# Optimization experiments

Hardware: AMD Instinct MI355X
Metric: run time of the kernel (lower is better)

Reference implementation:

```python
import jax, jax.numpy as jnp
import numpy as np

H = 256; NH = 4; DH = H // NH
NT, NS, NV = 4096, 2048, 1024
E1, E2, E3 = 65536, 16384, 32768
LN_EPS = 1e-5


def setup_inputs() -> dict:
    key = jax.random.key(0)
    ks = jax.random.split(key, 40)
    def nrm(i, shape):
        return jax.random.normal(ks[i], shape, jnp.float32) * 0.05
    inp = {
        "x_term": jax.random.normal(ks[0], (NT, H), jnp.float32),
        "x_symbol": jax.random.normal(ks[1], (NS, H), jnp.float32),
        "x_var": jax.random.normal(ks[2], (NV, H), jnp.float32),
        "ha_src": jax.random.randint(ks[3], (E1,), 0, NT),
        "ha_dst": jax.random.randint(ks[4], (E1,), 0, NT),
        "so_src": jax.random.randint(ks[5], (E2,), 0, NT),
        "so_dst": jax.random.randint(ks[6], (E2,), 0, NS),
        "vo_src": jax.random.randint(ks[7], (E3,), 0, NV),
        "vo_dst": jax.random.randint(ks[8], (E3,), 0, NT),
        # SAGEConv params for the 4 term-destination relations
        "Wl_rha": nrm(9, (H, H)),  "bl_rha": nrm(10, (H,)), "Wr_rha": nrm(11, (H, H)),
        "Wl_ha":  nrm(12, (H, H)), "bl_ha":  nrm(13, (H,)), "Wr_ha":  nrm(14, (H, H)),
        "Wl_rsym": nrm(15, (H, H)), "bl_rsym": nrm(16, (H,)), "Wr_rsym": nrm(17, (H, H)),
        "Wl_var": nrm(18, (H, H)), "bl_var": nrm(19, (H,)), "Wr_var": nrm(20, (H, H)),
        "ln_g": jnp.ones((H,), jnp.float32),
        "ln_b": jnp.zeros((H,), jnp.float32),
        "in_proj_w": nrm(21, (3 * H, H)),
        "in_proj_b": nrm(22, (3 * H,)),
        "out_proj_w": nrm(23, (H, H)),
        "out_proj_b": nrm(24, (H,)),
        "post_w": nrm(25, (H, H)),
        "post_b": nrm(26, (H,)),
    }
    return inp


def _sage(x_src, x_dst, src, dst, Wl, bl, Wr, num_dst):
    # PyG SAGEConv: lin_l(mean_j x_src[j]) + lin_r(x_dst)
    msg = x_src[src]                                            # [E, H] gather
    s = jax.ops.segment_sum(msg, dst, num_segments=num_dst)     # [N_dst, H] scatter-add
    cnt = jax.ops.segment_sum(jnp.ones((src.shape[0],), x_src.dtype), dst,
                              num_segments=num_dst)
    agg = s / jnp.maximum(cnt, 1.0)[:, None]
    return agg @ Wl.T + bl + x_dst @ Wr.T


def _layernorm(x, g, b):
    mu = jnp.mean(x, axis=-1, keepdims=True)
    var = jnp.mean(jnp.square(x - mu), axis=-1, keepdims=True)
    return (x - mu) * jax.lax.rsqrt(var + LN_EPS) * g + b


def _mha(x, in_w, in_b, out_w, out_b):
    # torch MultiheadAttention (eval, batch=1, self-attention)
    qkv = x @ in_w.T + in_b                       # [N, 3H]
    q, k, v = jnp.split(qkv, 3, axis=-1)
    def heads(t):
        return t.reshape(-1, NH, DH).transpose(1, 0, 2)  # [NH, N, DH]
    q, k, v = heads(q), heads(k), heads(v)
    scores = jnp.einsum("hqd,hkd->hqk", q, k) / np.sqrt(DH).astype(np.float32)
    a = jax.nn.softmax(scores, axis=-1)
    o = jnp.einsum("hqk,hkd->hqd", a, v)          # [NH, N, DH]
    o = o.transpose(1, 0, 2).reshape(-1, H)
    return o @ out_w.T + out_b


def reference(x_term, x_symbol, x_var,
              ha_src, ha_dst, so_src, so_dst, vo_src, vo_dst,
              Wl_rha, bl_rha, Wr_rha, Wl_ha, bl_ha, Wr_ha,
              Wl_rsym, bl_rsym, Wr_rsym, Wl_var, bl_var, Wr_var,
              ln_g, ln_b, in_proj_w, in_proj_b, out_proj_w, out_proj_b,
              post_w, post_b):
    nt = x_term.shape[0]
    # HeteroConv(aggr='sum') over the 4 relations whose destination is 'term'
    conv_term = (
        _sage(x_term, x_term, ha_dst, ha_src, Wl_rha, bl_rha, Wr_rha, nt)    # rev_has_arg
        + _sage(x_term, x_term, ha_src, ha_dst, Wl_ha, bl_ha, Wr_ha, nt)     # has_arg
        + _sage(x_symbol, x_term, so_dst, so_src, Wl_rsym, bl_rsym, Wr_rsym, nt)  # rev_symbol_of
        + _sage(x_var, x_term, vo_src, vo_dst, Wl_var, bl_var, Wr_var, nt)   # var_occurrence
    )
    term_out = _layernorm(conv_term + x_term, ln_g, ln_b)  # dropout is identity in eval
    attn_out = _mha(term_out, in_proj_w, in_proj_b, out_proj_w, out_proj_b)
    post = jax.nn.relu(attn_out @ post_w.T + post_b)
    term_final = post + term_out
    return term_final
```

## Files before the change

kernel.cpp:

```cpp
#include <hip/hip_runtime.h>
#include <hip/hip_bf16.h>

#define H 256
#define NT 4096
#define NHEAD 4
#define E1 65536
#define E2 16384
#define E3 32768
#define TOTE (2 * E1 + E2 + E3)
#define LN_EPS 1e-5f
#define SPLIT 4

typedef __hip_bfloat16 bf16;
typedef short bf16x8 __attribute__((ext_vector_type(8)));
typedef float f32x4 __attribute__((ext_vector_type(4)));

__device__ __forceinline__ float b2f(bf16 v) { return __bfloat162float(v); }
__device__ __forceinline__ float u2f(unsigned short u) {
    unsigned int x = ((unsigned int)u) << 16;
    return __uint_as_float(x);
}
__device__ __forceinline__ unsigned short f2u(float f) {
    bf16 h = __float2bfloat16(f);
    unsigned short v;
    __builtin_memcpy(&v, &h, 2);
    return v;
}
__device__ __forceinline__ float ldin(const void* p, size_t i, bool isbf) {
    return isbf ? b2f(((const bf16*)p)[i]) : ((const float*)p)[i];
}

__global__ __launch_bounds__(256) void k_init(float4* cnt4, int n4,
                                              const unsigned int* __restrict__ lng,
                                              unsigned int* __restrict__ flag) {
    int i = blockIdx.x * 256 + threadIdx.x;
    if (i == 0) *flag = (lng[0] == 0x3F803F80u) ? 1u : 0u;
    int stride = gridDim.x * 256;
    float4 z = make_float4(0.f, 0.f, 0.f, 0.f);
    for (; i < n4; i += stride) cnt4[i] = z;
}

__global__ __launch_bounds__(256) void k_count4(const int* __restrict__ s0, const int* __restrict__ s1,
                                                const int* __restrict__ s2, const int* __restrict__ s3,
                                                int* __restrict__ cnt) {
    int i = blockIdx.x * 256 + threadIdx.x;
    int r, e;
    if (i < E1) { r = 0; e = i; }
    else if (i < 2 * E1) { r = 1; e = i - E1; }
    else if (i < 2 * E1 + E2) { r = 2; e = i - 2 * E1; }
    else if (i < TOTE) { r = 3; e = i - 2 * E1 - E2; }
    else return;
    const int* s = (r == 0) ? s0 : (r == 1) ? s1 : (r == 2) ? s2 : s3;
    atomicAdd(&cnt[r * NT + s[e]], 1);
}

__global__ __launch_bounds__(256) void k_scan(const int* __restrict__ cnt, int* __restrict__ offs,
                                              int* __restrict__ cursor) {
    __shared__ int tot[256];
    int t = threadIdx.x, r = blockIdx.x;
    const int* c = cnt + r * NT;
    int* o = offs + r * (NT + 1);
    int* cur = cursor + r * NT;
    int base = t * 16;
    int local[16];
    int sum = 0;
#pragma unroll
    for (int j = 0; j < 16; j++) { local[j] = c[base + j]; sum += local[j]; }
    tot[t] = sum;
    __syncthreads();
    if (t == 0) {
        int run = 0;
        for (int i = 0; i < 256; i++) { int v = tot[i]; tot[i] = run; run += v; }
        o[NT] = run;
    }
    __syncthreads();
    int run = tot[t];
#pragma unroll
    for (int j = 0; j < 16; j++) { o[base + j] = run; cur[base + j] = run; run += local[j]; }
}

__global__ __launch_bounds__(256) void k_fill(const int* __restrict__ s0, const int* __restrict__ s1,
                                              const int* __restrict__ s2, const int* __restrict__ s3,
                                              const int* __restrict__ g0, const int* __restrict__ g1,
                                              const int* __restrict__ g2, const int* __restrict__ g3,
                                              int* __restrict__ cursor, int* __restrict__ csr) {
    int i = blockIdx.x * 256 + threadIdx.x;
    int r, e, rb;
    if (i < E1) { r = 0; e = i; rb = 0; }
    else if (i < 2 * E1) { r = 1; e = i - E1; rb = E1; }
    else if (i < 2 * E1 + E2) { r = 2; e = i - 2 * E1; rb = 2 * E1; }
    else if (i < TOTE) { r = 3; e = i - 2 * E1 - E2; rb = 2 * E1 + E2; }
    else return;
    const int* s = (r == 0) ? s0 : (r == 1) ? s1 : (r == 2) ? s2 : s3;
    const int* g = (r == 0) ? g0 : (r == 1) ? g1 : (r == 2) ? g2 : g3;
    int d = s[e];
    int pos = atomicAdd(&cursor[r * NT + d], 1);
    csr[rb + pos] = g[e];
}

__global__ __launch_bounds__(256) void k_gatherA(
    const void* __restrict__ x0, const void* __restrict__ x1,
    const void* __restrict__ x2, const void* __restrict__ x3,
    const int* __restrict__ offs, const int* __restrict__ csr,
    bf16* __restrict__ aggs, const unsigned int* __restrict__ flag) {
    int y = blockIdx.y;
    int i = blockIdx.x * 4 + (threadIdx.x >> 6);
    int lane = threadIdx.x & 63;
    bool isbf = (*flag != 0u);
    const void* x = (y == 0) ? x0 : (y == 1) ? x1 : (y == 2) ? x2 : x3;
    static const int rbase[4] = {0, E1, 2 * E1, 2 * E1 + E2};
    const int* o = offs + y * (NT + 1);
    const int* cs = csr + rbase[y];
    int b = o[i], e = o[i + 1];
    float ax = 0.f, ay = 0.f, az = 0.f, aw = 0.f;
    if (isbf) {
        for (int j = b; j < e; j++) {
            int s = cs[j];
            ushort4 u = *(const ushort4*)((const unsigned short*)x + (size_t)s * H + lane * 4);
            ax += u2f(u.x); ay += u2f(u.y); az += u2f(u.z); aw += u2f(u.w);
        }
    } else {
        for (int j = b; j < e; j++) {
            int s = cs[j];
            float4 v = *(const float4*)((const float*)x + (size_t)s * H + lane * 4);
            ax += v.x; ay += v.y; az += v.z; aw += v.w;
        }
    }
    float inv = 1.0f / fmaxf((float)(e - b), 1.0f);
    *(ushort4*)((unsigned short*)aggs + ((size_t)y * NT + i) * H + lane * 4) =
        make_ushort4(f2u(ax * inv), f2u(ay * inv), f2u(az * inv), f2u(aw * inv));
}

__global__ __launch_bounds__(256) void k_prepB(
    const void* __restrict__ Wl0, const void* __restrict__ Wl1,
    const void* __restrict__ Wl2, const void* __restrict__ Wl3,
    const void* __restrict__ Wr0, const void* __restrict__ Wr1,
    const void* __restrict__ Wr2, const void* __restrict__ Wr3,
    const void* __restrict__ b0, const void* __restrict__ b1,
    const void* __restrict__ b2, const void* __restrict__ b3,
    bf16* __restrict__ Bcat, float* __restrict__ bsum, const unsigned int* __restrict__ flag) {
    int idx = blockIdx.x * 256 + threadIdx.x;
    bool isbf = (*flag != 0u);
    int n = idx / 1280, k = idx % 1280;
    float v;
    if (k < 1024) {
        const void* W = (k < 256) ? Wl0 : (k < 512) ? Wl1 : (k < 768) ? Wl2 : Wl3;
        v = ldin(W, (size_t)n * 256 + (k & 255), isbf);
    } else {
        size_t o = (size_t)n * 256 + (k - 1024);
        v = ldin(Wr0, o, isbf) + ldin(Wr1, o, isbf) + ldin(Wr2, o, isbf) + ldin(Wr3, o, isbf);
    }
    ((unsigned short*)Bcat)[idx] = f2u(v);
    if (idx < 256)
        bsum[idx] = ldin(b0, idx, isbf) + ldin(b1, idx, isbf) + ldin(b2, idx, isbf) + ldin(b3, idx, isbf);
}

__global__ __launch_bounds__(256) void k_convln(
    const bf16* __restrict__ aggs, const bf16* __restrict__ Bcat, const float* __restrict__ bsum,
    const void* __restrict__ xt, const void* __restrict__ gw, const void* __restrict__ gb,
    bf16* __restrict__ term, const unsigned int* __restrict__ flag) {
    __shared__ unsigned short Asm[8 * 16 * 8];
    __shared__ unsigned short Bsm[8 * 256 * 8];
    __shared__ float redS[4][16];
    const bool isbf = (*flag != 0u);
    const int tid = threadIdx.x;
    const int w = tid >> 6, lane = tid & 63;
    const int col = lane & 15, quad = lane >> 4;
    const int m0 = blockIdx.x * 16;
    const int srow = tid & 63, skq = tid >> 6;

    f32x4 acc[4];
#pragma unroll
    for (int dt = 0; dt < 4; dt++) acc[dt] = (f32x4){0.f, 0.f, 0.f, 0.f};

    bf16x8 areg;
    bf16x8 breg[8];
    auto loadA = [&](int k0) {
        if (tid < 128) {
            int row = tid & 15, akq = tid >> 4;
            int k = k0 + akq * 8;
            if (k < 1024) {
                areg = *(const bf16x8*)((const unsigned short*)aggs +
                                        ((size_t)(k >> 8) * NT + m0 + row) * 256 + (k & 255));
            } else {
#pragma unroll
                for (int j = 0; j < 8; j++)
                    areg[j] = (short)f2u(ldin(xt, (size_t)(m0 + row) * 256 + (k - 1024) + j, isbf));
            }
        }
    };
    auto loadB = [&](int k0) {
#pragma unroll
        for (int t = 0; t < 4; t++)
#pragma unroll
            for (int kk = 0; kk < 2; kk++)
                breg[t * 2 + kk] = *(const bf16x8*)((const unsigned short*)Bcat +
                                       (size_t)(t * 64 + srow) * 1280 + k0 + (skq * 2 + kk) * 8);
    };

    loadA(0);
    loadB(0);
    for (int k0 = 0; k0 < 1280; k0 += 64) {
        __syncthreads();
        if (tid < 128) *(bf16x8*)&Asm[tid * 8] = areg;
#pragma unroll
        for (int t = 0; t < 4; t++)
#pragma unroll
            for (int kk = 0; kk < 2; kk++)
                *(bf16x8*)&Bsm[((skq * 2 + kk) * 256 + t * 64 + srow) * 8] = breg[t * 2 + kk];
        __syncthreads();
        if (k0 + 64 < 1280) { loadA(k0 + 64); loadB(k0 + 64); }
#pragma unroll
        for (int ch = 0; ch < 2; ch++) {
            bf16x8 a = *(const bf16x8*)&Asm[(((ch * 4 + quad) & 7) * 16 + col) * 8];
#pragma unroll
            for (int dt = 0; dt < 4; dt++) {
                bf16x8 b = *(const bf16x8*)&Bsm[((ch * 4 + quad) * 256 + w * 64 + dt * 16 + col) * 8];
                acc[dt] = __builtin_amdgcn_mfma_f32_16x16x32_bf16(a, b, acc[dt], 0, 0, 0);
            }
        }
    }

#pragma unroll
    for (int dt = 0; dt < 4; dt++) {
        int n = w * 64 + dt * 16 + col;
        float bsv = bsum[n];
#pragma unroll
        for (int r = 0; r < 4; r++) {
            int m = m0 + quad * 4 + r;
            acc[dt][r] += bsv + ldin(xt, (size_t)m * 256 + n, isbf);
        }
    }
    float mu[4], rs_[4];
#pragma unroll
    for (int r = 0; r < 4; r++) {
        float s = acc[0][r] + acc[1][r] + acc[2][r] + acc[3][r];
#pragma unroll
        for (int mk = 1; mk <= 8; mk <<= 1) s += __shfl_xor(s, mk);
        if (col == 0) redS[w][quad * 4 + r] = s;
    }
    __syncthreads();
#pragma unroll
    for (int r = 0; r < 4; r++) {
        int m = quad * 4 + r;
        mu[r] = (redS[0][m] + redS[1][m] + redS[2][m] + redS[3][m]) * (1.0f / 256.0f);
    }
    __syncthreads();
#pragma unroll
    for (int r = 0; r < 4; r++) {
        float s2 = 0.f;
#pragma unroll
        for (int dt = 0; dt < 4; dt++) {
            float d = acc[dt][r] - mu[r];
            s2 += d * d;
        }
#pragma unroll
        for (int mk = 1; mk <= 8; mk <<= 1) s2 += __shfl_xor(s2, mk);
        if (col == 0) redS[w][quad * 4 + r] = s2;
    }
    __syncthreads();
#pragma unroll
    for (int r = 0; r < 4; r++) {
        int m = quad * 4 + r;
        float var = (redS[0][m] + redS[1][m] + redS[2][m] + redS[3][m]) * (1.0f / 256.0f);
        rs_[r] = rsqrtf(var + LN_EPS);
    }
#pragma unroll
    for (int dt = 0; dt < 4; dt++) {
        int n = w * 64 + dt * 16 + col;
        float gv = ldin(gw, n, isbf), bv = ldin(gb, n, isbf);
#pragma unroll
        for (int r = 0; r < 4; r++) {
            int m = m0 + quad * 4 + r;
            term[(size_t)m * 256 + n] = __float2bfloat16((acc[dt][r] - mu[r]) * rs_[r] * gv + bv);
        }
    }
}

template <int AMODE, int EPI>
__global__ __launch_bounds__(256) void k_gemm(
    const void* __restrict__ A, const void* __restrict__ A2, const float* __restrict__ ml,
    const void* __restrict__ B, const void* __restrict__ bias,
    const bf16* __restrict__ resid, bf16* __restrict__ vt, void* __restrict__ outp,
    int M, int N, int K, const unsigned int* __restrict__ flag) {
    __shared__ unsigned short Asm[8 * 64 * 8];
    __shared__ unsigned short Bsm[8 * 64 * 8];
    const bool isbf = (*flag != 0u);
    const int tid = threadIdx.x;
    const int w = tid >> 6, lane = tid & 63;
    const int col = lane & 15, quad = lane >> 4;
    const int m0 = blockIdx.x * 64, n0 = blockIdx.y * 64;
    const int srow = tid & 63, skq = tid >> 6;
    const int am = m0 + srow;

    f32x4 acc[4];
#pragma unroll
    for (int dt = 0; dt < 4; dt++) acc[dt] = (f32x4){0.f, 0.f, 0.f, 0.f};

    bf16x8 areg[2], breg[2];
    auto loadA = [&](int k0) {
#pragma unroll
        for (int c = 0; c < 2; c++) {
            int k = k0 + skq * 16 + c * 8;
            if (AMODE == 0) {
                areg[c] = *(const bf16x8*)((const unsigned short*)A + (size_t)am * K + k);
            } else {
                int h = k >> 6;
                float l0 = ml[(size_t)(0 * NHEAD + h) * NT + am];
                float l1 = ml[(size_t)(1 * NHEAD + h) * NT + am];
                float l2 = ml[(size_t)(2 * NHEAD + h) * NT + am];
                float l3 = ml[(size_t)(3 * NHEAD + h) * NT + am];
                float iw = 1.0f / (l0 + l1 + l2 + l3);
                bf16x8 o0 = *(const bf16x8*)((const unsigned short*)A + (size_t)am * H + k);
                bf16x8 o1 = *(const bf16x8*)((const unsigned short*)A + ((size_t)NT + am) * H + k);
                bf16x8 o2 = *(const bf16x8*)((const unsigned short*)A2 + (size_t)am * H + k);
                bf16x8 o3 = *(const bf16x8*)((const unsigned short*)A2 + ((size_t)NT + am) * H + k);
#pragma unroll
                for (int j = 0; j < 8; j++)
                    areg[c][j] = (short)f2u((l0 * u2f((unsigned short)o0[j]) + l1 * u2f((unsigned short)o1[j]) +
                                             l2 * u2f((unsigned short)o2[j]) + l3 * u2f((unsigned short)o3[j])) * iw);
            }
        }
    };
    auto loadB = [&](int k0) {
#pragma unroll
        for (int c = 0; c < 2; c++) {
            size_t bi = (size_t)(n0 + srow) * K + k0 + skq * 16 + c * 8;
            if (isbf) {
                breg[c] = *(const bf16x8*)((const unsigned short*)B + bi);
            } else {
#pragma unroll
                for (int j = 0; j < 8; j++) breg[c][j] = (short)f2u(((const float*)B)[bi + j]);
            }
        }
    };

    loadA(0);
    loadB(0);
    for (int k0 = 0; k0 < K; k0 += 64) {
        __syncthreads();
#pragma unroll
        for (int c = 0; c < 2; c++) {
            *(bf16x8*)&Asm[((skq * 2 + c) * 64 + srow) * 8] = areg[c];
            *(bf16x8*)&Bsm[((skq * 2 + c) * 64 + srow) * 8] = breg[c];
        }
        __syncthreads();
        if (k0 + 64 < K) { loadA(k0 + 64); loadB(k0 + 64); }
#pragma unroll
        for (int ch = 0; ch < 2; ch++) {
            bf16x8 a = *(const bf16x8*)&Asm[((ch * 4 + quad) * 64 + w * 16 + col) * 8];
#pragma unroll
            for (int dt = 0; dt < 4; dt++) {
                bf16x8 b = *(const bf16x8*)&Bsm[((ch * 4 + quad) * 64 + dt * 16 + col) * 8];
                acc[dt] = __builtin_amdgcn_mfma_f32_16x16x32_bf16(a, b, acc[dt], 0, 0, 0);
            }
        }
    }
#pragma unroll
    for (int dt = 0; dt < 4; dt++) {
        int n = n0 + dt * 16 + col;
        float bv = ldin(bias, n, isbf);
        if (EPI == 3 && n0 >= 512) {
            int m = m0 + w * 16 + quad * 4;
            *(ushort4*)((unsigned short*)vt + (size_t)(n - 512) * NT + m) =
                make_ushort4(f2u(acc[dt][0] + bv), f2u(acc[dt][1] + bv),
                             f2u(acc[dt][2] + bv), f2u(acc[dt][3] + bv));
            continue;
        }
#pragma unroll
        for (int r = 0; r < 4; r++) {
            int m = m0 + w * 16 + quad * 4 + r;
            float v = acc[dt][r] + bv;
            if (EPI == 3) {
                ((bf16*)outp)[(size_t)m * 512 + n] = __float2bfloat16(v);
            } else if (EPI == 2) {
                size_t off = (size_t)m * N + n;
                v = fmaxf(v, 0.f);
                v += b2f(resid[off]);
                ((float*)outp)[off] = v;
            } else {
                ((bf16*)outp)[(size_t)m * N + n] = __float2bfloat16(v);
            }
        }
    }
}

__global__ __launch_bounds__(256) void k_attn(const bf16* __restrict__ qkvQK,
                                              const bf16* __restrict__ vt,
                                              bf16* __restrict__ opart01,
                                              bf16* __restrict__ opart23,
                                              float* __restrict__ ml) {
    __shared__ unsigned short Ksm[8 * 64 * 8];
    __shared__ unsigned short Vsm[8 * 64 * 8];
    const int h = blockIdx.y, sp = blockIdx.z;
    const int q0 = blockIdx.x * 64;
    const int tid = threadIdx.x;
    const int w = tid >> 6, lane = tid & 63;
    const int col = lane & 15, quad = lane >> 4;
    const unsigned short* qk = (const unsigned short*)qkvQK;
    const unsigned short* vp = (const unsigned short*)vt;

    bf16x8 aQ[2];
#pragma unroll
    for (int ch = 0; ch < 2; ch++)
        aQ[ch] = *(const bf16x8*)(qk + (size_t)(q0 + w * 16 + col) * 512 +
                                  h * 64 + ch * 32 + quad * 8);

    f32x4 O[4];
#pragma unroll
    for (int dt = 0; dt < 4; dt++) O[dt] = (f32x4){0.f, 0.f, 0.f, 0.f};
    float lsum = 0.f;

    const int kbeg = sp * (NT / SPLIT), kend = kbeg + NT / SPLIT;
    const float SC = 0.125f * 1.44269504f;

    bf16x8 kreg[2], vreg[2];
    auto loadKV = [&](int kb) {
#pragma unroll
        for (int it = 0; it < 2; it++) {
            int cid = tid + it * 256;
            int kkey = cid & 63, dhq = cid >> 6;
            kreg[it] = *(const bf16x8*)(qk + (size_t)(kb + kkey) * 512 + 256 + h * 64 + dhq * 8);
            int vd = cid & 63, vo = cid >> 6;
            vreg[it] = *(const bf16x8*)(vp + (size_t)(h * 64 + vd) * NT + kb + vo * 8);
        }
    };
    loadKV(kbeg);

    for (int kb = kbeg; kb < kend; kb += 64) {
        __syncthreads();
#pragma unroll
        for (int it = 0; it < 2; it++) {
            int cid = tid + it * 256;
            *(bf16x8*)&Ksm[cid * 8] = kreg[it];
            *(bf16x8*)&Vsm[cid * 8] = vreg[it];
        }
        __syncthreads();
        if (kb + 64 < kend) loadKV(kb + 64);

        f32x4 c[4];
        __builtin_amdgcn_s_setprio(1);
#pragma unroll
        for (int dt = 0; dt < 4; dt++) {
            c[dt] = (f32x4){0.f, 0.f, 0.f, 0.f};
#pragma unroll
            for (int ch = 0; ch < 2; ch++) {
                bf16x8 kf = *(const bf16x8*)&Ksm[((ch * 4 + quad) * 64 + dt * 16 + col) * 8];
                c[dt] = __builtin_amdgcn_mfma_f32_16x16x32_bf16(kf, aQ[ch], c[dt], 0, 0, 0);
            }
        }
        __builtin_amdgcn_s_setprio(0);

        float pp[4][4];
#pragma unroll
        for (int dt = 0; dt < 4; dt++) {
#pragma unroll
            for (int r = 0; r < 4; r++) {
                pp[dt][r] = __builtin_amdgcn_exp2f(c[dt][r] * SC);
            }
            lsum += (pp[dt][0] + pp[dt][1]) + (pp[dt][2] + pp[dt][3]);
        }

        union PU { unsigned int u[4]; bf16x8 v; };
        PU ap[2];
#pragma unroll
        for (int kc = 0; kc < 2; kc++) {
            unsigned int a0, a1, b0, b1;
            asm("v_cvt_pk_bf16_f32 %0, %1, %2" : "=v"(a0) : "v"(pp[2 * kc][0]), "v"(pp[2 * kc][1]));
            asm("v_cvt_pk_bf16_f32 %0, %1, %2" : "=v"(a1) : "v"(pp[2 * kc][2]), "v"(pp[2 * kc][3]));
            asm("v_cvt_pk_bf16_f32 %0, %1, %2" : "=v"(b0) : "v"(pp[2 * kc + 1][0]), "v"(pp[2 * kc + 1][1]));
            asm("v_cvt_pk_bf16_f32 %0, %1, %2" : "=v"(b1) : "v"(pp[2 * kc + 1][2]), "v"(pp[2 * kc + 1][3]));
            asm("v_permlane32_swap_b32 %0, %1" : "+v"(a0), "+v"(b0));
            asm("v_permlane16_swap_b32 %0, %1" : "+v"(a0), "+v"(b0));
            asm("v_permlane32_swap_b32 %0, %1" : "+v"(a1), "+v"(b1));
            asm("v_permlane16_swap_b32 %0, %1" : "+v"(a1), "+v"(b1));
            ap[kc].u[0] = a0; ap[kc].u[1] = a1; ap[kc].u[2] = b0; ap[kc].u[3] = b1;
        }

        __builtin_amdgcn_s_setprio(1);
#pragma unroll
        for (int dt = 0; dt < 4; dt++)
#pragma unroll
            for (int kc = 0; kc < 2; kc++) {
                bf16x8 b = *(const bf16x8*)&Vsm[((kc * 4 + quad) * 64 + dt * 16 + col) * 8];
                O[dt] = __builtin_amdgcn_mfma_f32_16x16x32_bf16(ap[kc].v, b, O[dt], 0, 0, 0);
            }
        __builtin_amdgcn_s_setprio(0);
    }
    float l = lsum;
    l += __shfl_xor(l, 16);
    l += __shfl_xor(l, 32);
    bf16* ob = (sp < 2) ? (opart01 + (size_t)sp * NT * H) : (opart23 + (size_t)(sp - 2) * NT * H);
    if (quad == 0)
        ml[((size_t)sp * NHEAD + h) * NT + (q0 + w * 16 + col)] = l;
    float lr[4];
#pragma unroll
    for (int r = 0; r < 4; r++) lr[r] = __shfl(l, quad * 4 + r, 16);
#pragma unroll
    for (int dt = 0; dt < 4; dt++) {
#pragma unroll
        for (int r = 0; r < 4; r++) {
            int q = q0 + w * 16 + quad * 4 + r;
            ob[(size_t)q * H + h * 64 + dt * 16 + col] = __float2bfloat16(O[dt][r] / lr[r]);
        }
    }
}

extern "C" void kernel_launch(void* const* d_in, const int* in_sizes, int n_in,
                              void* d_out, int out_size, void* d_ws, size_t ws_size,
                              hipStream_t stream) {
    const void* x_term   = d_in[0];
    const void* x_symbol = d_in[1];
    const void* x_var    = d_in[2];
    const int* ha_src = (const int*)d_in[3];
    const int* ha_dst = (const int*)d_in[4];
    const int* so_src = (const int*)d_in[5];
    const int* so_dst = (const int*)d_in[6];
    const int* vo_src = (const int*)d_in[7];
    const int* vo_dst = (const int*)d_in[8];
    const void* Wl[4]  = {d_in[9],  d_in[12], d_in[15], d_in[18]};
    const void* blv[4] = {d_in[10], d_in[13], d_in[16], d_in[19]};
    const void* Wr[4]  = {d_in[11], d_in[14], d_in[17], d_in[20]};
    const void* ln_g = d_in[21];
    const void* ln_b = d_in[22];
    const void* in_w = d_in[23];
    const void* in_b = d_in[24];
    const void* out_w = d_in[25];
    const void* out_b = d_in[26];
    const void* post_w = d_in[27];
    const void* post_b = d_in[28];

    char* ws = (char*)d_ws;
    unsigned int* flag = (unsigned int*)ws;
    char* csrbase = ws + 256;
    int* cnt    = (int*)csrbase;
    int* offs   = (int*)(csrbase + 65536);
    int* cursor = (int*)(csrbase + 132096);
    int* csr    = (int*)(csrbase + 197632);
    bf16*  Bcat = (bf16*)csrbase;
    float* bsum = (float*)(csrbase + 655360);
    float* ml   = (float*)csrbase;
    bf16* aggs  = (bf16*)(ws + (1 << 20));
    bf16* term  = (bf16*)(ws + (1 << 20) + 8388608);
    bf16* opart23 = (bf16*)(ws + (1 << 20) + 10485760);
    bf16* qkvQK = aggs;
    bf16* vt    = (bf16*)((char*)aggs + 4194304);
    bf16* proj  = aggs;
    bf16* opart01 = (bf16*)d_out;

    k_init<<<16, 256, 0, stream>>>((float4*)cnt, 4 * NT / 4, (const unsigned int*)ln_g, flag);
    k_count4<<<(TOTE + 255) / 256, 256, 0, stream>>>(ha_src, ha_dst, so_src, vo_dst, cnt);
    k_scan<<<4, 256, 0, stream>>>(cnt, offs, cursor);
    k_fill<<<(TOTE + 255) / 256, 256, 0, stream>>>(ha_src, ha_dst, so_src, vo_dst,
                                                   ha_dst, ha_src, so_dst, vo_src, cursor, csr);
    k_gatherA<<<dim3(NT / 4, 4), 256, 0, stream>>>(x_term, x_term, x_symbol, x_var,
                                                   offs, csr, aggs, flag);
    k_prepB<<<(256 * 1280) / 256, 256, 0, stream>>>(Wl[0], Wl[1], Wl[2], Wl[3],
                                                    Wr[0], Wr[1], Wr[2], Wr[3],
                                                    blv[0], blv[1], blv[2], blv[3],
                                                    Bcat, bsum, flag);

    k_convln<<<256, 256, 0, stream>>>(aggs, Bcat, bsum, x_term, ln_g, ln_b, term, flag);

    k_gemm<0, 3><<<dim3(64, 12), 256, 0, stream>>>(
        term, nullptr, nullptr, in_w, in_b, nullptr, vt, qkvQK, NT, 768, 256, flag);

    k_attn<<<dim3(64, NHEAD, SPLIT), 256, 0, stream>>>(qkvQK, vt, opart01, opart23, ml);

    k_gemm<1, 0><<<dim3(64, 4), 256, 0, stream>>>(
        opart01, opart23, ml, out_w, out_b, nullptr, nullptr, proj, NT, 256, 256, flag);

    k_gemm<0, 2><<<dim3(64, 4), 256, 0, stream>>>(
        proj, nullptr, nullptr, post_w, post_b, term, nullptr, d_out, NT, 256, 256, flag);

    (void)in_sizes; (void)n_in; (void)out_size; (void)ws_size;
}
```

Before: 275.8 us.

## Double-buffer attention K/V tiles with direct global-to-LDS loads

The attention kernel now stages K and V tiles straight from global memory into LDS using global_load_lds, with two LDS buffers. The next tile is prefetched into the alternate buffer while MFMAs run on the current one. This drops the register round-trip and one barrier per iteration. It doubles LDS use per block, and correctness relies on the single barrier plus the implicit wait before LDS reads. That could be a race if the compiler does not insert vmcnt waits for the async LDS loads.

```diff
diff --git a/kernel.cpp b/kernel.cpp
--- a/kernel.cpp
+++ b/kernel.cpp
@@ -28,6 +28,11 @@
 }
 __device__ __forceinline__ float ldin(const void* p, size_t i, bool isbf) {
     return isbf ? b2f(((const bf16*)p)[i]) : ((const float*)p)[i];
+}
+__device__ __forceinline__ void gload_lds16(const void* g, void* l) {
+    __builtin_amdgcn_global_load_lds(
+        (const __attribute__((address_space(1))) unsigned int*)g,
+        (__attribute__((address_space(3))) unsigned int*)l, 16, 0, 0);
 }
 
 __global__ __launch_bounds__(256) void k_init(float4* cnt4, int n4,
@@ -390,8 +395,8 @@
                                               bf16* __restrict__ opart01,
                                               bf16* __restrict__ opart23,
                                               float* __restrict__ ml) {
-    __shared__ unsigned short Ksm[8 * 64 * 8];
-    __shared__ unsigned short Vsm[8 * 64 * 8];
+    __shared__ unsigned short Ksm[2][8 * 64 * 8];
+    __shared__ unsigned short Vsm[2][8 * 64 * 8];
     const int h = blockIdx.y, sp = blockIdx.z;
     const int q0 = blockIdx.x * 64;
     const int tid = threadIdx.x;
@@ -414,29 +419,22 @@
     const int kbeg = sp * (NT / SPLIT), kend = kbeg + NT / SPLIT;
     const float SC = 0.125f * 1.44269504f;
 
-    bf16x8 kreg[2], vreg[2];
-    auto loadKV = [&](int kb) {
+    auto stage = [&](int kb, int buf) {
 #pragma unroll
         for (int it = 0; it < 2; it++) {
-            int cid = tid + it * 256;
-            int kkey = cid & 63, dhq = cid >> 6;
-            kreg[it] = *(const bf16x8*)(qk + (size_t)(kb + kkey) * 512 + 256 + h * 64 + dhq * 8);
-            int vd = cid & 63, vo = cid >> 6;
-            vreg[it] = *(const bf16x8*)(vp + (size_t)(h * 64 + vd) * NT + kb + vo * 8);
+            int dhq = it * 4 + w;
+            gload_lds16(qk + (size_t)(kb + lane) * 512 + 256 + h * 64 + dhq * 8,
+                        &Ksm[buf][(it * 256 + w * 64) * 8]);
+            gload_lds16(vp + (size_t)(h * 64 + lane) * NT + kb + dhq * 8,
+                        &Vsm[buf][(it * 256 + w * 64) * 8]);
         }
     };
-    loadKV(kbeg);
-
+
+    stage(kbeg, 0);
+    __syncthreads();
+    int cur = 0;
     for (int kb = kbeg; kb < kend; kb += 64) {
-        __syncthreads();
-#pragma unroll
-        for (int it = 0; it < 2; it++) {
-            int cid = tid + it * 256;
-            *(bf16x8*)&Ksm[cid * 8] = kreg[it];
-            *(bf16x8*)&Vsm[cid * 8] = vreg[it];
-        }
-        __syncthreads();
-        if (kb + 64 < kend) loadKV(kb + 64);
+        if (kb + 64 < kend) stage(kb + 64, cur ^ 1);
 
         f32x4 c[4];
         __builtin_amdgcn_s_setprio(1);
@@ -445,7 +443,7 @@
             c[dt] = (f32x4){0.f, 0.f, 0.f, 0.f};
 #pragma unroll
             for (int ch = 0; ch < 2; ch++) {
-                bf16x8 kf = *(const bf16x8*)&Ksm[((ch * 4 + quad) * 64 + dt * 16 + col) * 8];
+                bf16x8 kf = *(const bf16x8*)&Ksm[cur][((ch * 4 + quad) * 64 + dt * 16 + col) * 8];
                 c[dt] = __builtin_amdgcn_mfma_f32_16x16x32_bf16(kf, aQ[ch], c[dt], 0, 0, 0);
             }
         }
@@ -482,10 +480,13 @@
         for (int dt = 0; dt < 4; dt++)
 #pragma unroll
             for (int kc = 0; kc < 2; kc++) {
-                bf16x8 b = *(const bf16x8*)&Vsm[((kc * 4 + quad) * 64 + dt * 16 + col) * 8];
+                bf16x8 b = *(const bf16x8*)&Vsm[cur][((kc * 4 + quad) * 64 + dt * 16 + col) * 8];
                 O[dt] = __builtin_amdgcn_mfma_f32_16x16x32_bf16(ap[kc].v, b, O[dt], 0, 0, 0);
             }
         __builtin_amdgcn_s_setprio(0);
+
+        __syncthreads();
+        cur ^= 1;
     }
     float l = lsum;
     l += __shfl_xor(l, 16);
```

New measurement: 276.7 us. No clear change (+0.3%).
